# Kernel optimization log

Measured on AMD Instinct MI355X. Metric: run time of the kernel, lower is better.

The kernel has to match this reference:

```python
import jax, jax.numpy as jnp
import numpy as np

B, S, D, H = 2, 2048, 1024, 16
DK = D // H


def setup_inputs() -> dict:
    key = jax.random.key(0)
    ks = jax.random.split(key, 7)
    q = jax.random.normal(ks[0], (B, S, D), dtype=jnp.float32)
    k = jax.random.normal(ks[1], (B, S, D), dtype=jnp.float32)
    v = jax.random.normal(ks[2], (B, S, D), dtype=jnp.float32)
    # causal mask: mask==0 positions get -1e9 before softmax
    mask = jnp.tril(jnp.ones((S, S), dtype=jnp.int32))[None, None, :, :]
    scale = 0.02
    w_q = jax.random.normal(ks[3], (D, D), dtype=jnp.float32) * scale
    w_k = jax.random.normal(ks[4], (D, D), dtype=jnp.float32) * scale
    w_v = jax.random.normal(ks[5], (D, D), dtype=jnp.float32) * scale
    w_o = jax.random.normal(ks[6], (D, D), dtype=jnp.float32) * scale
    return {"q": q, "k": k, "v": v, "mask": mask,
            "w_q": w_q, "w_k": w_k, "w_v": w_v, "w_o": w_o}


def reference(q, k, v, mask, w_q, w_k, w_v, w_o):
    # nn.Linear(bias=False): x @ W.T
    query = q @ w_q.T  # [B,S,D]
    key = k @ w_k.T
    value = v @ w_v.T
    # split heads -> [B,H,S,DK]
    query = query.reshape(B, S, H, DK).transpose(0, 2, 1, 3)
    key = key.reshape(B, S, H, DK).transpose(0, 2, 1, 3)
    value = value.reshape(B, S, H, DK).transpose(0, 2, 1, 3)
    scores = jnp.einsum('bhqd,bhkd->bhqk', query, key) / jnp.sqrt(
        jnp.asarray(DK, dtype=query.dtype))
    scores = jnp.where(mask == 0, jnp.asarray(-1e9, scores.dtype), scores)
    attn = jax.nn.softmax(scores, axis=-1)  # dropout p=0.0 -> identity
    x = jnp.einsum('bhqk,bhkd->bhqd', attn, value)  # [B,H,S,DK]
    x = x.transpose(0, 2, 1, 3).reshape(B, S, D)
    return x @ w_o.T
```

## Files before the change

kernel.cpp:

```cpp
#include <hip/hip_runtime.h>

typedef __attribute__((ext_vector_type(8))) short short8;
typedef __attribute__((ext_vector_type(4))) float f32x4;

#define DEVI static __device__ __forceinline__

constexpr int BB = 2, SS = 2048, DD = 1024, HH = 16, DKK = 64;
constexpr size_t QN = (size_t)BB * SS * DD;
constexpr size_t WN = (size_t)DD * DD;

constexpr size_t OFF_WQ = 3 * QN;
constexpr size_t OFF_WO = OFF_WQ + 3 * WN;
constexpr size_t OFF_QM = OFF_WQ + 4 * WN;
constexpr size_t OFF_KM = OFF_QM + QN;
constexpr size_t OFF_VM = OFF_QM + 2 * QN;
constexpr size_t OFF_XC = OFF_QM + 3 * QN;

DEVI unsigned short f2bf(float f) {
  unsigned int u = __float_as_uint(f);
  u = (u + 0x7fffu + ((u >> 16) & 1u)) >> 16;
  return (unsigned short)u;
}

DEVI f32x4 fzero() { f32x4 z = {0.f, 0.f, 0.f, 0.f}; return z; }

DEVI void gld16(const void* g, void* l) {
  __builtin_amdgcn_global_load_lds((__attribute__((address_space(1))) void*)g,
                                   (__attribute__((address_space(3))) void*)l,
                                   16, 0, 0);
}

DEVI short8 mk8u(unsigned int a, unsigned int b, unsigned int c, unsigned int d) {
  union { short8 s; unsigned int u[4]; } x;
  x.u[0] = a; x.u[1] = b; x.u[2] = c; x.u[3] = d;
  return x.s;
}

DEVI short8 mk8q(unsigned long long lo, unsigned long long hi) {
  union { short8 s; unsigned long long q[2]; } x;
  x.q[0] = lo; x.q[1] = hi;
  return x.s;
}

DEVI unsigned int pkbf(float a, float b) {
  return __builtin_amdgcn_perm(__float_as_uint(b), __float_as_uint(a), 0x07060302u);
}

#define VMBAR(N) asm volatile("s_waitcnt vmcnt(" #N ")\n\ts_barrier" ::: "memory")
#define LGKM0                                      \
  do {                                             \
    asm volatile("s_waitcnt lgkmcnt(0)" ::: "memory"); \
    __builtin_amdgcn_sched_barrier(0);             \
  } while (0)

__global__ __launch_bounds__(256) void convert_all(
    const float* __restrict__ q, const float* __restrict__ k,
    const float* __restrict__ v, const float* __restrict__ wq,
    const float* __restrict__ wk, const float* __restrict__ wv,
    const float* __restrict__ wo, unsigned short* __restrict__ ws) {
  size_t t = (size_t)blockIdx.x * 256 + threadIdx.x;
  size_t e = t * 4;
  const float* src;
  size_t base, idx;
  if (e < 3 * QN) {
    size_t a = e >> 22;
    idx = e & (QN - 1);
    src = (a == 0) ? q : (a == 1) ? k : v;
    base = a * QN;
  } else {
    size_t r = e - 3 * QN;
    size_t a = r >> 20;
    idx = r & (WN - 1);
    src = (a == 0) ? wq : (a == 1) ? wk : (a == 2) ? wv : wo;
    base = 3 * QN + a * WN;
  }
  float4 f = *(const float4*)(src + idx);
  ushort4 o;
  o.x = f2bf(f.x); o.y = f2bf(f.y); o.z = f2bf(f.z); o.w = f2bf(f.w);
  *(ushort4*)(ws + base + idx) = o;
}

__global__ __launch_bounds__(512, 2) void proj_gemm(unsigned short* __restrict__ ws) {
  __shared__ unsigned short lds[65536];
  const int tid = threadIdx.x;
  const int w = tid >> 6, l = tid & 63;
  const int lr = l & 15, qd = l >> 4, l7 = l & 7, l3 = l >> 3;
  const int wr = w >> 2, wc = w & 3;

  const int orig = blockIdx.x;
  const int swz = (orig & 7) * 24 + (orig >> 3);
  const int mt = swz >> 2, nt = swz & 3;
  const int z = mt >> 4;
  const int m0 = (mt & 15) * 256, n0 = nt * 256;

  const unsigned short* Ab = ws + (size_t)z * QN;
  const unsigned short* Wb = ws + OFF_WQ + (size_t)z * WN;
  unsigned short* O = ws + OFF_QM + (size_t)z * QN;

  const bool vz = (z == 2);
  const unsigned short* src0 = vz ? Ab : Wb;
  const unsigned short* src1 = vz ? Wb : Ab;
  const int base0 = vz ? m0 : n0;
  const int base1 = vz ? n0 : m0;

  f32x4 acc[8][4];
#pragma unroll
  for (int i = 0; i < 8; ++i)
#pragma unroll
    for (int j = 0; j < 4; ++j) acc[i][j] = fzero();

  auto stage = [&](int buf, int ab, int h, int kt) {
    const unsigned short* src = ab ? src1 : src0;
    const int rc0 = (ab ? base1 : base0) + h * 128 + w * 8 + l3;
    const int kofs = kt * 64 + ((l7 ^ l3) * 8);
    unsigned short* d = &lds[buf * 32768 + ab * 16384 + h * 8192 + w * 512];
#pragma unroll
    for (int u = 0; u < 2; ++u)
      gld16(src + (size_t)(rc0 + u * 64) * DD + kofs, d + u * 4096);
  };
  auto rdA = [&](int buf, int fi, int ks) -> short8 {
    const int rg = (fi * 2 + wr) * 16 + lr;
    const int c2 = (ks * 4 + qd) ^ l7;
    return *(const short8*)&lds[buf * 32768 + rg * 64 + c2 * 8];
  };
  auto rdB = [&](int buf, int fj, int ks) -> short8 {
    const int rg = (fj * 4 + wc) * 16 + lr;
    const int c2 = (ks * 4 + qd) ^ l7;
    return *(const short8*)&lds[buf * 32768 + 16384 + rg * 64 + c2 * 8];
  };

  stage(0, 0, 0, 0);
  stage(0, 1, 0, 0);
  stage(0, 1, 1, 0);
  stage(0, 0, 1, 0);

  constexpr int NT = DD / 64;
#pragma unroll 1
  for (int t = 0; t < NT; ++t) {
    const int rb = t & 1, wb = rb ^ 1;
    const bool g = (t + 1 < NT);
    short8 af[4][2], bf[2][2], bh[2][2];

    VMBAR(4);
    if (g) stage(wb, 0, 0, t + 1);
#pragma unroll
    for (int mi = 0; mi < 4; ++mi)
#pragma unroll
      for (int ks = 0; ks < 2; ++ks) af[mi][ks] = rdA(rb, mi, ks);
#pragma unroll
    for (int nj = 0; nj < 2; ++nj)
#pragma unroll
      for (int ks = 0; ks < 2; ++ks) bf[nj][ks] = rdB(rb, nj, ks);
    LGKM0;
    __builtin_amdgcn_s_setprio(1);
#pragma unroll
    for (int mi = 0; mi < 4; ++mi)
#pragma unroll
      for (int nj = 0; nj < 2; ++nj)
#pragma unroll
        for (int ks = 0; ks < 2; ++ks)
          acc[mi][nj] = __builtin_amdgcn_mfma_f32_16x16x32_bf16(
              af[mi][ks], bf[nj][ks], acc[mi][nj], 0, 0, 0);
    __builtin_amdgcn_s_setprio(0);

    if (g) { VMBAR(4); } else { VMBAR(2); }
    if (g) stage(wb, 1, 0, t + 1);
#pragma unroll
    for (int nj = 0; nj < 2; ++nj)
#pragma unroll
      for (int ks = 0; ks < 2; ++ks) bh[nj][ks] = rdB(rb, 2 + nj, ks);
    LGKM0;
    __builtin_amdgcn_s_setprio(1);
#pragma unroll
    for (int mi = 0; mi < 4; ++mi)
#pragma unroll
      for (int nj = 0; nj < 2; ++nj)
#pragma unroll
        for (int ks = 0; ks < 2; ++ks)
          acc[mi][2 + nj] = __builtin_amdgcn_mfma_f32_16x16x32_bf16(
              af[mi][ks], bh[nj][ks], acc[mi][2 + nj], 0, 0, 0);
    __builtin_amdgcn_s_setprio(0);

    if (g) { VMBAR(4); } else { VMBAR(0); }
    if (g) stage(wb, 1, 1, t + 1);
#pragma unroll
    for (int mi = 0; mi < 4; ++mi)
#pragma unroll
      for (int ks = 0; ks < 2; ++ks) af[mi][ks] = rdA(rb, 4 + mi, ks);
    LGKM0;
    __builtin_amdgcn_s_setprio(1);
#pragma unroll
    for (int mi = 0; mi < 4; ++mi)
#pragma unroll
      for (int nj = 0; nj < 2; ++nj)
#pragma unroll
        for (int ks = 0; ks < 2; ++ks)
          acc[4 + mi][nj] = __builtin_amdgcn_mfma_f32_16x16x32_bf16(
              af[mi][ks], bf[nj][ks], acc[4 + mi][nj], 0, 0, 0);
    __builtin_amdgcn_s_setprio(0);

    if (g) stage(wb, 0, 1, t + 1);
    __builtin_amdgcn_s_setprio(1);
#pragma unroll
    for (int mi = 0; mi < 4; ++mi)
#pragma unroll
      for (int nj = 0; nj < 2; ++nj)
#pragma unroll
        for (int ks = 0; ks < 2; ++ks)
          acc[4 + mi][2 + nj] = __builtin_amdgcn_mfma_f32_16x16x32_bf16(
              af[mi][ks], bh[nj][ks], acc[4 + mi][2 + nj], 0, 0, 0);
    __builtin_amdgcn_s_setprio(0);
  }

  if (vz) {
#pragma unroll
    for (int fi = 0; fi < 8; ++fi)
#pragma unroll
      for (int fj = 0; fj < 4; ++fj) {
        const int n = n0 + (fj * 4 + wc) * 16 + lr;
        const int h = n >> 6, dk = n & 63;
        const int m = m0 + (fi * 2 + wr) * 16 + qd * 4;
        const int b = m >> 11, s = m & 2047;
        ushort4 pk;
        pk.x = f2bf(acc[fi][fj][0]); pk.y = f2bf(acc[fi][fj][1]);
        pk.z = f2bf(acc[fi][fj][2]); pk.w = f2bf(acc[fi][fj][3]);
        *(ushort4*)&O[((size_t)(b * HH + h) * DKK + dk) * SS + s] = pk;
      }
  } else {
#pragma unroll
    for (int fi = 0; fi < 8; ++fi)
#pragma unroll
      for (int fj = 0; fj < 4; ++fj) {
        const int nb = n0 + (fi * 2 + wr) * 16 + qd * 4;
        const int h = nb >> 6, dk = nb & 63;
        const int m = m0 + (fj * 4 + wc) * 16 + lr;
        const int b = m >> 11, s = m & 2047;
        ushort4 pk;
        pk.x = f2bf(acc[fi][fj][0]); pk.y = f2bf(acc[fi][fj][1]);
        pk.z = f2bf(acc[fi][fj][2]); pk.w = f2bf(acc[fi][fj][3]);
        *(ushort4*)&O[((size_t)(b * HH + h) * SS + s) * DKK + dk] = pk;
      }
  }
}

__global__ __launch_bounds__(512) void flash_attn(
    const unsigned short* __restrict__ Qm, const unsigned short* __restrict__ Km,
    const unsigned short* __restrict__ Vt, unsigned short* __restrict__ Xc) {
  __shared__ unsigned short sh[32768];
  unsigned short* KA = sh;
  unsigned short* VA = sh + 8192;
  unsigned short* KL = sh + 16384;
  unsigned short* VL = sh + 24576;

  const int head = blockIdx.x, py = blockIdx.y, b = blockIdx.z;
  const int p = b ? 15 - py : py;
  const int tid = threadIdx.x, w = tid >> 6, l = tid & 63, lr = l & 15, qd = l >> 4;
  const int slr = lr ^ ((lr >> 3) << 2);
  const size_t bh = (size_t)(b * HH + head);
  const unsigned short* Qb = Qm + bh * SS * DKK;
  const unsigned short* Kb = Km + bh * SS * DKK;
  const unsigned short* Vb = Vt + bh * DKK * SS;

  const bool heavy = (w < 4);
  const int g = w & 3;
  const int At = 31 - p, Bt = p;
  const int s0 = g, s1 = g + 4;
  const int loOff = ((qd >> 1) * 16 + slr) * 8 + (qd & 1) * 4;
  const int hiOff = ((2 + (qd >> 1)) * 16 + slr) * 8 + (qd & 1) * 4;

  int qrow = (heavy ? At : Bt) * 64 + g * 16 + lr;
  short8 qf0 = *(const short8*)&Qb[(size_t)qrow * DKK + qd * 8];
  short8 qf1 = *(const short8*)&Qb[(size_t)qrow * DKK + 32 + qd * 8];

  f32x4 o[4];
#pragma unroll
  for (int i = 0; i < 4; ++i) o[i] = fzero();
  float ll = 0.f;
  const float c1 = 0.18033688011112042f;
  const float mc = 8.0f * c1;

  auto stK = [&](unsigned short* dst, int buf, int kv) {
    unsigned short* d = dst + buf * 4096;
    gld16(&Kb[(size_t)(kv * 64 + (s0 >> 1) * 16 + lr) * DKK + (s0 & 1) * 32 + qd * 8],
          d + s0 * 512);
    gld16(&Kb[(size_t)(kv * 64 + (s1 >> 1) * 16 + lr) * DKK + (s1 & 1) * 32 + qd * 8],
          d + s1 * 512);
  };
  auto stV = [&](unsigned short* dst, int buf, int kv) {
    unsigned short* d = dst + buf * 4096;
    gld16(&Vb[(size_t)((s0 >> 1) * 16 + slr) * SS + kv * 64 + (s0 & 1) * 32 + qd * 8],
          d + s0 * 512);
    gld16(&Vb[(size_t)((s1 >> 1) * 16 + slr) * SS + kv * 64 + (s1 & 1) * 32 + qd * 8],
          d + s1 * 512);
  };

  auto body = [&](const unsigned short* Kc, const unsigned short* Vc,
                  int kv, int myqt) {
    const int kv0 = kv * 64;
    short8 kf0[4], kf1[4];
#pragma unroll
    for (int nt = 0; nt < 4; ++nt) {
      kf0[nt] = *(const short8*)&Kc[(nt * 2 + 0) * 512 + l * 8];
      kf1[nt] = *(const short8*)&Kc[(nt * 2 + 1) * 512 + l * 8];
    }
    f32x4 sc[4];
    __builtin_amdgcn_s_setprio(1);
#pragma unroll
    for (int nt = 0; nt < 4; ++nt) {
      f32x4 zz = fzero();
      zz = __builtin_amdgcn_mfma_f32_16x16x32_bf16(kf0[nt], qf0, zz, 0, 0, 0);
      sc[nt] = __builtin_amdgcn_mfma_f32_16x16x32_bf16(kf1[nt], qf1, zz, 0, 0, 0);
    }
    __builtin_amdgcn_s_setprio(0);
    if (kv == myqt) {
#pragma unroll
      for (int nt = 0; nt < 4; ++nt)
#pragma unroll
        for (int i = 0; i < 4; ++i) {
          const int kvi = kv0 + nt * 16 + qd * 4 + i;
          if (kvi > qrow) sc[nt][i] = -3e38f;
        }
    }
#pragma unroll
    for (int nt = 0; nt < 4; ++nt)
#pragma unroll
      for (int i = 0; i < 4; ++i) {
        const float pp = exp2f(fmaf(sc[nt][i], c1, -mc));
        sc[nt][i] = pp;
        ll += pp;
      }
    unsigned int pd[4][2];
#pragma unroll
    for (int f = 0; f < 4; ++f) {
      pd[f][0] = pkbf(sc[f][0], sc[f][1]);
      pd[f][1] = pkbf(sc[f][2], sc[f][3]);
    }
#pragma unroll
    for (int kh = 0; kh < 2; ++kh) {
      short8 bfr = mk8u(pd[2 * kh][0], pd[2 * kh][1],
                        pd[2 * kh + 1][0], pd[2 * kh + 1][1]);
      unsigned long long vlo[4], vhi[4];
#pragma unroll
      for (int mt = 0; mt < 4; ++mt) {
        const int sbase = (mt * 2 + kh) * 512;
        vlo[mt] = *(const unsigned long long*)&Vc[sbase + loOff];
        vhi[mt] = *(const unsigned long long*)&Vc[sbase + hiOff];
      }
      __builtin_amdgcn_s_setprio(1);
#pragma unroll
      for (int mt = 0; mt < 4; ++mt)
        o[mt] = __builtin_amdgcn_mfma_f32_16x16x32_bf16(mk8q(vlo[mt], vhi[mt]),
                                                        bfr, o[mt], 0, 0, 0);
      __builtin_amdgcn_s_setprio(0);
    }
  };

  if (heavy) { stK(KA, 0, 0); stV(VA, 0, 0); }

#pragma unroll 1
  for (int t = 0; t <= 16; ++t) {
    __syncthreads();
    const int cura = t & 1;
    if (heavy) {
      if (t < 16) { stK(KA, cura ^ 1, t + 1); stV(VA, cura ^ 1, t + 1); }
      body(KA + cura * 4096, VA + cura * 4096, t, At);
    } else {
      if (t >= p && t + 1 <= 15) {
        const int kvn = t + 17 - p;
        const int bufn = (t - p) & 1;
        stK(KL, bufn, kvn);
        stV(VL, bufn, kvn);
      }
      if (t <= 15) {
        const bool ph1 = (t <= p);
        const int kv = ph1 ? t : t + 16 - p;
        const int myqt = ph1 ? Bt : At;
        const unsigned short* Kc =
            ph1 ? (KA + cura * 4096) : (KL + ((t - p - 1) & 1) * 4096);
        const unsigned short* Vc =
            ph1 ? (VA + cura * 4096) : (VL + ((t - p - 1) & 1) * 4096);
        body(Kc, Vc, kv, myqt);
        if (t == p) {
          float llB = ll;
          llB += __shfl_xor(llB, 16);
          llB += __shfl_xor(llB, 32);
          const float invB = 1.0f / llB;
          unsigned short* Xr =
              Xc + ((size_t)b * SS + qrow) * DD + (size_t)head * DKK;
#pragma unroll
          for (int mt = 0; mt < 4; ++mt)
#pragma unroll
            for (int i = 0; i < 4; ++i)
              Xr[mt * 16 + qd * 4 + i] = f2bf(o[mt][i] * invB);
#pragma unroll
          for (int i = 0; i < 4; ++i) o[i] = fzero();
          ll = 0.f;
          qrow = At * 64 + g * 16 + lr;
          qf0 = *(const short8*)&Qb[(size_t)qrow * DKK + qd * 8];
          qf1 = *(const short8*)&Qb[(size_t)qrow * DKK + 32 + qd * 8];
        }
      }
    }
  }

  __syncthreads();
  float* shp = (float*)sh;
  const int pbase = (g * 64 + l) * 17;
  if (!heavy) {
#pragma unroll
    for (int mt = 0; mt < 4; ++mt)
#pragma unroll
      for (int i = 0; i < 4; ++i) shp[pbase + mt * 4 + i] = o[mt][i];
    shp[pbase + 16] = ll;
  }
  __syncthreads();
  if (heavy) {
#pragma unroll
    for (int mt = 0; mt < 4; ++mt)
#pragma unroll
      for (int i = 0; i < 4; ++i) o[mt][i] += shp[pbase + mt * 4 + i];
    ll += shp[pbase + 16];
    ll += __shfl_xor(ll, 16);
    ll += __shfl_xor(ll, 32);
    const float inv = 1.0f / ll;
    unsigned short* Xr = Xc + ((size_t)b * SS + qrow) * DD + (size_t)head * DKK;
#pragma unroll
    for (int mt = 0; mt < 4; ++mt)
#pragma unroll
      for (int i = 0; i < 4; ++i)
        Xr[mt * 16 + qd * 4 + i] = f2bf(o[mt][i] * inv);
  }
}

__global__ __launch_bounds__(256, 2) void out_gemm(
    const unsigned short* __restrict__ Xc, const unsigned short* __restrict__ Wo,
    float* __restrict__ out) {
  __shared__ unsigned short lds[32768];
  const int tid = threadIdx.x;
  const int w = tid >> 6, l = tid & 63;
  const int lr = l & 15, qd = l >> 4, l7 = l & 7, l3 = l >> 3;
  const int wr = w >> 1, wc = w & 1;
  const int m0 = blockIdx.x * 128, n0 = blockIdx.y * 128;

  f32x4 acc[4][4];
#pragma unroll
  for (int i = 0; i < 4; ++i)
#pragma unroll
    for (int j = 0; j < 4; ++j) acc[i][j] = fzero();

  auto stage = [&](int buf, int ab, int h, int kt) {
    const unsigned short* src = ab ? Wo : Xc;
    const int rc0 = (ab ? n0 : m0) + h * 64 + w * 8 + l3;
    const int kofs = kt * 64 + ((l7 ^ l3) * 8);
    unsigned short* d = &lds[buf * 16384 + ab * 8192 + h * 4096 + w * 512];
#pragma unroll
    for (int u = 0; u < 2; ++u)
      gld16(src + (size_t)(rc0 + u * 32) * DD + kofs, d + u * 2048);
  };
  auto rdA = [&](int buf, int mf, int ks) -> short8 {
    const int rg = mf * 16 + lr;
    const int c2 = (ks * 4 + qd) ^ l7;
    return *(const short8*)&lds[buf * 16384 + rg * 64 + c2 * 8];
  };
  auto rdB = [&](int buf, int nf, int ks) -> short8 {
    const int rg = nf * 16 + lr;
    const int c2 = (ks * 4 + qd) ^ l7;
    return *(const short8*)&lds[buf * 16384 + 8192 + rg * 64 + c2 * 8];
  };

  stage(0, 0, 0, 0);
  stage(0, 1, 0, 0);
  stage(0, 1, 1, 0);
  stage(0, 0, 1, 0);

  constexpr int NT = DD / 64;
#pragma unroll 1
  for (int t = 0; t < NT; ++t) {
    const int rb = t & 1, wb = rb ^ 1;
    const bool g = (t + 1 < NT);
    short8 af[2][2], bf[2][2], bh[2][2];

    VMBAR(4);
    if (g) stage(wb, 0, 0, t + 1);
#pragma unroll
    for (int mi = 0; mi < 2; ++mi)
#pragma unroll
      for (int ks = 0; ks < 2; ++ks) af[mi][ks] = rdA(rb, mi * 2 + wr, ks);
#pragma unroll
    for (int nj = 0; nj < 2; ++nj)
#pragma unroll
      for (int ks = 0; ks < 2; ++ks) bf[nj][ks] = rdB(rb, nj * 2 + wc, ks);
    LGKM0;
    __builtin_amdgcn_s_setprio(1);
#pragma unroll
    for (int mi = 0; mi < 2; ++mi)
#pragma unroll
      for (int nj = 0; nj < 2; ++nj)
#pragma unroll
        for (int ks = 0; ks < 2; ++ks)
          acc[mi][nj] = __builtin_amdgcn_mfma_f32_16x16x32_bf16(
              af[mi][ks], bf[nj][ks], acc[mi][nj], 0, 0, 0);
    __builtin_amdgcn_s_setprio(0);

    if (g) { VMBAR(4); } else { VMBAR(2); }
    if (g) stage(wb, 1, 0, t + 1);
#pragma unroll
    for (int nj = 0; nj < 2; ++nj)
#pragma unroll
      for (int ks = 0; ks < 2; ++ks) bh[nj][ks] = rdB(rb, (2 + nj) * 2 + wc, ks);
    LGKM0;
    __builtin_amdgcn_s_setprio(1);
#pragma unroll
    for (int mi = 0; mi < 2; ++mi)
#pragma unroll
      for (int nj = 0; nj < 2; ++nj)
#pragma unroll
        for (int ks = 0; ks < 2; ++ks)
          acc[mi][2 + nj] = __builtin_amdgcn_mfma_f32_16x16x32_bf16(
              af[mi][ks], bh[nj][ks], acc[mi][2 + nj], 0, 0, 0);
    __builtin_amdgcn_s_setprio(0);

    if (g) { VMBAR(4); } else { VMBAR(0); }
    if (g) stage(wb, 1, 1, t + 1);
#pragma unroll
    for (int mi = 0; mi < 2; ++mi)
#pragma unroll
      for (int ks = 0; ks < 2; ++ks) af[mi][ks] = rdA(rb, (2 + mi) * 2 + wr, ks);
    LGKM0;
    __builtin_amdgcn_s_setprio(1);
#pragma unroll
    for (int mi = 0; mi < 2; ++mi)
#pragma unroll
      for (int nj = 0; nj < 2; ++nj)
#pragma unroll
        for (int ks = 0; ks < 2; ++ks)
          acc[2 + mi][nj] = __builtin_amdgcn_mfma_f32_16x16x32_bf16(
              af[mi][ks], bf[nj][ks], acc[2 + mi][nj], 0, 0, 0);
    __builtin_amdgcn_s_setprio(0);

    if (g) stage(wb, 0, 1, t + 1);
    __builtin_amdgcn_s_setprio(1);
#pragma unroll
    for (int mi = 0; mi < 2; ++mi)
#pragma unroll
      for (int nj = 0; nj < 2; ++nj)
#pragma unroll
        for (int ks = 0; ks < 2; ++ks)
          acc[2 + mi][2 + nj] = __builtin_amdgcn_mfma_f32_16x16x32_bf16(
              af[mi][ks], bh[nj][ks], acc[2 + mi][2 + nj], 0, 0, 0);
    __builtin_amdgcn_s_setprio(0);
  }

#pragma unroll
  for (int a = 0; a < 4; ++a)
#pragma unroll
    for (int c = 0; c < 4; ++c) {
      const int n = n0 + (c * 2 + wc) * 16 + lr;
#pragma unroll
      for (int i = 0; i < 4; ++i) {
        const int m = m0 + (a * 2 + wr) * 16 + qd * 4 + i;
        out[(size_t)m * DD + n] = acc[a][c][i];
      }
    }
}

extern "C" void kernel_launch(void* const* d_in, const int* in_sizes, int n_in,
                              void* d_out, int out_size, void* d_ws, size_t ws_size,
                              hipStream_t stream) {
  (void)in_sizes; (void)n_in; (void)out_size; (void)ws_size;
  const float* q  = (const float*)d_in[0];
  const float* k  = (const float*)d_in[1];
  const float* v  = (const float*)d_in[2];
  const float* wq = (const float*)d_in[4];
  const float* wk = (const float*)d_in[5];
  const float* wv = (const float*)d_in[6];
  const float* wo = (const float*)d_in[7];
  unsigned short* ws = (unsigned short*)d_ws;
  float* out = (float*)d_out;

  convert_all<<<dim3(16384), dim3(256), 0, stream>>>(q, k, v, wq, wk, wv, wo, ws);
  proj_gemm<<<dim3(192), dim3(512), 0, stream>>>(ws);
  flash_attn<<<dim3(16, 16, 2), dim3(512), 0, stream>>>(ws + OFF_QM, ws + OFF_KM,
                                                        ws + OFF_VM, ws + OFF_XC);
  out_gemm<<<dim3(32, 8), dim3(256), 0, stream>>>(ws + OFF_XC, ws + OFF_WO, out);
}
```

Before: 218.7 us.

## Shrink projection GEMM tiles to 128x128 with triple-buffered K=32 pipeline

```diff
diff --git a/kernel.cpp b/kernel.cpp
--- a/kernel.cpp
+++ b/kernel.cpp
@@ -80,18 +80,18 @@
   *(ushort4*)(ws + base + idx) = o;
 }
 
-__global__ __launch_bounds__(512, 2) void proj_gemm(unsigned short* __restrict__ ws) {
-  __shared__ unsigned short lds[65536];
+__global__ __launch_bounds__(256, 3) void proj_gemm(unsigned short* __restrict__ ws) {
+  __shared__ unsigned short lds[24576];
   const int tid = threadIdx.x;
   const int w = tid >> 6, l = tid & 63;
-  const int lr = l & 15, qd = l >> 4, l7 = l & 7, l3 = l >> 3;
-  const int wr = w >> 2, wc = w & 3;
+  const int lr = l & 15, qd = l >> 4;
+  const int wr = w >> 1, wc = w & 1;
 
   const int orig = blockIdx.x;
-  const int swz = (orig & 7) * 24 + (orig >> 3);
-  const int mt = swz >> 2, nt = swz & 3;
-  const int z = mt >> 4;
-  const int m0 = (mt & 15) * 256, n0 = nt * 256;
+  const int swz = (orig & 7) * 96 + (orig >> 3);
+  const int mt = swz >> 3, nt = swz & 7;
+  const int z = mt >> 5;
+  const int m0 = (mt & 31) * 128, n0 = nt * 128;
 
   const unsigned short* Ab = ws + (size_t)z * QN;
   const unsigned short* Wb = ws + OFF_WQ + (size_t)z * WN;
@@ -103,141 +103,124 @@
   const int base0 = vz ? m0 : n0;
   const int base1 = vz ? n0 : m0;
 
-  f32x4 acc[8][4];
-#pragma unroll
-  for (int i = 0; i < 8; ++i)
+  f32x4 acc[4][4];
+#pragma unroll
+  for (int i = 0; i < 4; ++i)
 #pragma unroll
     for (int j = 0; j < 4; ++j) acc[i][j] = fzero();
 
   auto stage = [&](int buf, int ab, int h, int kt) {
     const unsigned short* src = ab ? src1 : src0;
-    const int rc0 = (ab ? base1 : base0) + h * 128 + w * 8 + l3;
-    const int kofs = kt * 64 + ((l7 ^ l3) * 8);
-    unsigned short* d = &lds[buf * 32768 + ab * 16384 + h * 8192 + w * 512];
-#pragma unroll
-    for (int u = 0; u < 2; ++u)
-      gld16(src + (size_t)(rc0 + u * 64) * DD + kofs, d + u * 4096);
-  };
-  auto rdA = [&](int buf, int fi, int ks) -> short8 {
-    const int rg = (fi * 2 + wr) * 16 + lr;
-    const int c2 = (ks * 4 + qd) ^ l7;
-    return *(const short8*)&lds[buf * 32768 + rg * 64 + c2 * 8];
-  };
-  auto rdB = [&](int buf, int fj, int ks) -> short8 {
-    const int rg = (fj * 4 + wc) * 16 + lr;
-    const int c2 = (ks * 4 + qd) ^ l7;
-    return *(const short8*)&lds[buf * 32768 + 16384 + rg * 64 + c2 * 8];
-  };
-
-  stage(0, 0, 0, 0);
-  stage(0, 1, 0, 0);
-  stage(0, 1, 1, 0);
-  stage(0, 0, 1, 0);
-
-  constexpr int NT = DD / 64;
+    const int row = (ab ? base1 : base0) + h * 64 + w * 16 + (l >> 2);
+    const int kofs = kt * 32 + (((l & 3) ^ ((l >> 3) & 3)) * 8);
+    gld16(src + (size_t)row * DD + kofs,
+          &lds[buf * 8192 + ab * 4096 + h * 2048 + w * 512]);
+  };
+  auto rdA = [&](int buf, int mf) -> short8 {
+    const int rg = mf * 16 + lr;
+    const int c2 = qd ^ ((lr >> 1) & 3);
+    return *(const short8*)&lds[buf * 8192 + rg * 32 + c2 * 8];
+  };
+  auto rdB = [&](int buf, int nf) -> short8 {
+    const int rg = nf * 16 + lr;
+    const int c2 = qd ^ ((lr >> 1) & 3);
+    return *(const short8*)&lds[buf * 8192 + 4096 + rg * 32 + c2 * 8];
+  };
+
+  stage(0, 0, 0, 0); stage(0, 1, 0, 0); stage(0, 1, 1, 0); stage(0, 0, 1, 0);
+  stage(1, 0, 0, 1); stage(1, 1, 0, 1); stage(1, 1, 1, 1); stage(1, 0, 1, 1);
+
+  constexpr int NT = DD / 32;
+  int rb = 0, wb = 2;
 #pragma unroll 1
   for (int t = 0; t < NT; ++t) {
-    const int rb = t & 1, wb = rb ^ 1;
-    const bool g = (t + 1 < NT);
-    short8 af[4][2], bf[2][2], bh[2][2];
-
-    VMBAR(4);
-    if (g) stage(wb, 0, 0, t + 1);
-#pragma unroll
-    for (int mi = 0; mi < 4; ++mi)
-#pragma unroll
-      for (int ks = 0; ks < 2; ++ks) af[mi][ks] = rdA(rb, mi, ks);
-#pragma unroll
-    for (int nj = 0; nj < 2; ++nj)
-#pragma unroll
-      for (int ks = 0; ks < 2; ++ks) bf[nj][ks] = rdB(rb, nj, ks);
+    const bool g = (t + 2 < NT);
+    short8 afl[2], bfl[2], afh[2], bfh[2];
+
+    if (t < NT - 1) { VMBAR(6); } else { VMBAR(2); }
+    if (g) stage(wb, 0, 0, t + 2);
+#pragma unroll
+    for (int a = 0; a < 2; ++a) afl[a] = rdA(rb, a * 2 + wr);
+#pragma unroll
+    for (int c = 0; c < 2; ++c) bfl[c] = rdB(rb, c * 2 + wc);
     LGKM0;
     __builtin_amdgcn_s_setprio(1);
 #pragma unroll
-    for (int mi = 0; mi < 4; ++mi)
-#pragma unroll
-      for (int nj = 0; nj < 2; ++nj)
-#pragma unroll
-        for (int ks = 0; ks < 2; ++ks)
-          acc[mi][nj] = __builtin_amdgcn_mfma_f32_16x16x32_bf16(
-              af[mi][ks], bf[nj][ks], acc[mi][nj], 0, 0, 0);
-    __builtin_amdgcn_s_setprio(0);
-
-    if (g) { VMBAR(4); } else { VMBAR(2); }
-    if (g) stage(wb, 1, 0, t + 1);
-#pragma unroll
-    for (int nj = 0; nj < 2; ++nj)
-#pragma unroll
-      for (int ks = 0; ks < 2; ++ks) bh[nj][ks] = rdB(rb, 2 + nj, ks);
+    for (int a = 0; a < 2; ++a)
+#pragma unroll
+      for (int c = 0; c < 2; ++c)
+        acc[a][c] = __builtin_amdgcn_mfma_f32_16x16x32_bf16(
+            afl[a], bfl[c], acc[a][c], 0, 0, 0);
+    __builtin_amdgcn_s_setprio(0);
+
+    if (t < NT - 2) { VMBAR(6); } else if (t == NT - 2) { VMBAR(5); } else { VMBAR(1); }
+    if (g) stage(wb, 1, 0, t + 2);
+#pragma unroll
+    for (int c = 0; c < 2; ++c) bfh[c] = rdB(rb, (2 + c) * 2 + wc);
     LGKM0;
     __builtin_amdgcn_s_setprio(1);
 #pragma unroll
-    for (int mi = 0; mi < 4; ++mi)
-#pragma unroll
-      for (int nj = 0; nj < 2; ++nj)
-#pragma unroll
-        for (int ks = 0; ks < 2; ++ks)
-          acc[mi][2 + nj] = __builtin_amdgcn_mfma_f32_16x16x32_bf16(
-              af[mi][ks], bh[nj][ks], acc[mi][2 + nj], 0, 0, 0);
-    __builtin_amdgcn_s_setprio(0);
-
-    if (g) { VMBAR(4); } else { VMBAR(0); }
-    if (g) stage(wb, 1, 1, t + 1);
-#pragma unroll
-    for (int mi = 0; mi < 4; ++mi)
-#pragma unroll
-      for (int ks = 0; ks < 2; ++ks) af[mi][ks] = rdA(rb, 4 + mi, ks);
+    for (int a = 0; a < 2; ++a)
+#pragma unroll
+      for (int c = 0; c < 2; ++c)
+        acc[a][2 + c] = __builtin_amdgcn_mfma_f32_16x16x32_bf16(
+            afl[a], bfh[c], acc[a][2 + c], 0, 0, 0);
+    __builtin_amdgcn_s_setprio(0);
+
+    if (t < NT - 2) { VMBAR(6); } else if (t == NT - 2) { VMBAR(4); } else { VMBAR(0); }
+    if (g) stage(wb, 1, 1, t + 2);
+#pragma unroll
+    for (int a = 0; a < 2; ++a) afh[a] = rdA(rb, (2 + a) * 2 + wr);
     LGKM0;
     __builtin_amdgcn_s_setprio(1);
 #pragma unroll
-    for (int mi = 0; mi < 4; ++mi)
-#pragma unroll
-      for (int nj = 0; nj < 2; ++nj)
-#pragma unroll
-        for (int ks = 0; ks < 2; ++ks)
-          acc[4 + mi][nj] = __builtin_amdgcn_mfma_f32_16x16x32_bf16(
-              af[mi][ks], bf[nj][ks], acc[4 + mi][nj], 0, 0, 0);
-    __builtin_amdgcn_s_setprio(0);
-
-    if (g) stage(wb, 0, 1, t + 1);
-    __builtin_amdgcn_s_setprio(1);
-#pragma unroll
-    for (int mi = 0; mi < 4; ++mi)
-#pragma unroll
-      for (int nj = 0; nj < 2; ++nj)
-#pragma unroll
-        for (int ks = 0; ks < 2; ++ks)
-          acc[4 + mi][2 + nj] = __builtin_amdgcn_mfma_f32_16x16x32_bf16(
-              af[mi][ks], bh[nj][ks], acc[4 + mi][2 + nj], 0, 0, 0);
-    __builtin_amdgcn_s_setprio(0);
+    for (int a = 0; a < 2; ++a)
+#pragma unroll
+      for (int c = 0; c < 2; ++c)
+        acc[2 + a][c] = __builtin_amdgcn_mfma_f32_16x16x32_bf16(
+            afh[a], bfl[c], acc[2 + a][c], 0, 0, 0);
+    __builtin_amdgcn_s_setprio(0);
+
+    if (g) stage(wb, 0, 1, t + 2);
+    __builtin_amdgcn_s_setprio(1);
+#pragma unroll
+    for (int a = 0; a < 2; ++a)
+#pragma unroll
+      for (int c = 0; c < 2; ++c)
+        acc[2 + a][2 + c] = __builtin_amdgcn_mfma_f32_16x16x32_bf16(
+            afh[a], bfh[c], acc[2 + a][2 + c], 0, 0, 0);
+    __builtin_amdgcn_s_setprio(0);
+
+    rb = (rb == 2) ? 0 : rb + 1;
+    wb = (wb == 2) ? 0 : wb + 1;
   }
 
   if (vz) {
 #pragma unroll
-    for (int fi = 0; fi < 8; ++fi)
-#pragma unroll
-      for (int fj = 0; fj < 4; ++fj) {
-        const int n = n0 + (fj * 4 + wc) * 16 + lr;
+    for (int a = 0; a < 4; ++a)
+#pragma unroll
+      for (int c = 0; c < 4; ++c) {
+        const int n = n0 + (c * 2 + wc) * 16 + lr;
         const int h = n >> 6, dk = n & 63;
-        const int m = m0 + (fi * 2 + wr) * 16 + qd * 4;
+        const int m = m0 + (a * 2 + wr) * 16 + qd * 4;
         const int b = m >> 11, s = m & 2047;
         ushort4 pk;
-        pk.x = f2bf(acc[fi][fj][0]); pk.y = f2bf(acc[fi][fj][1]);
-        pk.z = f2bf(acc[fi][fj][2]); pk.w = f2bf(acc[fi][fj][3]);
+        pk.x = f2bf(acc[a][c][0]); pk.y = f2bf(acc[a][c][1]);
+        pk.z = f2bf(acc[a][c][2]); pk.w = f2bf(acc[a][c][3]);
         *(ushort4*)&O[((size_t)(b * HH + h) * DKK + dk) * SS + s] = pk;
       }
   } else {
 #pragma unroll
-    for (int fi = 0; fi < 8; ++fi)
-#pragma unroll
-      for (int fj = 0; fj < 4; ++fj) {
-        const int nb = n0 + (fi * 2 + wr) * 16 + qd * 4;
+    for (int a = 0; a < 4; ++a)
+#pragma unroll
+      for (int c = 0; c < 4; ++c) {
+        const int nb = n0 + (a * 2 + wr) * 16 + qd * 4;
         const int h = nb >> 6, dk = nb & 63;
-        const int m = m0 + (fj * 4 + wc) * 16 + lr;
+        const int m = m0 + (c * 2 + wc) * 16 + lr;
         const int b = m >> 11, s = m & 2047;
         ushort4 pk;
-        pk.x = f2bf(acc[fi][fj][0]); pk.y = f2bf(acc[fi][fj][1]);
-        pk.z = f2bf(acc[fi][fj][2]); pk.w = f2bf(acc[fi][fj][3]);
+        pk.x = f2bf(acc[a][c][0]); pk.y = f2bf(acc[a][c][1]);
+        pk.z = f2bf(acc[a][c][2]); pk.w = f2bf(acc[a][c][3]);
         *(ushort4*)&O[((size_t)(b * HH + h) * SS + s) * DKK + dk] = pk;
       }
   }
@@ -579,7 +562,7 @@
   float* out = (float*)d_out;
 
   convert_all<<<dim3(16384), dim3(256), 0, stream>>>(q, k, v, wq, wk, wv, wo, ws);
-  proj_gemm<<<dim3(192), dim3(512), 0, stream>>>(ws);
+  proj_gemm<<<dim3(768), dim3(256), 0, stream>>>(ws);
   flash_attn<<<dim3(16, 16, 2), dim3(512), 0, stream>>>(ws + OFF_QM, ws + OFF_KM,
                                                         ws + OFF_VM, ws + OFF_XC);
   out_gemm<<<dim3(32, 8), dim3(256), 0, stream>>>(ws + OFF_XC, ws + OFF_WO, out);
```

Result: no change. 216.5 us (median of 2 runs) (-1.0%).
